# Kernel tuning notes

Hardware: AMD Instinct MI355X
Metric: run time of the kernel (lower is better)

Reference implementation:

```python
import jax, jax.numpy as jnp
import numpy as np

EPS = 1e-8  # torch F.cosine_similarity default eps


def setup_inputs() -> dict:
    key = jax.random.key(0)
    k1, k2 = jax.random.split(key)
    xs_pad = jax.random.normal(k1, (8, 8192, 256), dtype=jnp.float32)   # [B, T, D]
    spk_emb = jax.random.normal(k2, (8, 200, 256), dtype=jnp.float32)   # [B, S, D]
    return {"xs_pad": xs_pad, "spk_emb": spk_emb}


def reference(xs_pad, spk_emb):
    # Pairwise cosine similarity: [B, T, S]
    # Equivalent to F.cosine_similarity(xs.unsqueeze(2), spk.unsqueeze(1), dim=-1)
    # = dot(x, y) / max(||x|| * ||y||, eps)
    dot = jnp.einsum("btd,bsd->bts", xs_pad, spk_emb)
    nx = jnp.linalg.norm(xs_pad, axis=-1)    # [B, T]
    ny = jnp.linalg.norm(spk_emb, axis=-1)   # [B, S]
    denom = jnp.maximum(nx[:, :, None] * ny[:, None, :], EPS)
    return dot / denom
```

## Files before the change

### kernel.cpp

```cpp
#include <hip/hip_runtime.h>
#include <math.h>

typedef __attribute__((ext_vector_type(8))) _Float16 f16x8;
typedef __attribute__((ext_vector_type(4))) float f32x4;

#define BT 8192
#define BS 200
#define SP 208
#define DD 256
#define TM 128
#define LSTR 40
#define NJ 13

__global__ __launch_bounds__(256, 2)
void cos_scorer_kernel(const float* __restrict__ X, const float* __restrict__ SPK,
                       float* __restrict__ OUT) {
    const int b   = blockIdx.y;
    const int t0  = blockIdx.x * TM;
    const int tid = threadIdx.x;
    const int wid = tid >> 6;
    const int lane = tid & 63;
    const int lr  = lane & 15;
    const int lg  = lane >> 4;

    __shared__ _Float16 Shi[SP * LSTR];
    __shared__ _Float16 Slo[SP * LSTR];
    __shared__ float sn_l[SP];

    const float* __restrict__ spk_b = SPK + (size_t)b * BS * DD;

    const float* __restrict__ xrow0 = X + ((size_t)b * BT + t0 + wid * 32 + lr) * DD;
    const float* __restrict__ xrow1 = xrow0 + 16 * DD;

    float4 pa00 = *(const float4*)(xrow0 + lg * 8);
    float4 pa01 = *(const float4*)(xrow0 + lg * 8 + 4);
    float4 pa10 = *(const float4*)(xrow1 + lg * 8);
    float4 pa11 = *(const float4*)(xrow1 + lg * 8 + 4);

    if (tid < SP) {
        float ss = 0.f;
        if (tid < BS) {
            const float4* p = (const float4*)(spk_b + tid * DD);
            #pragma unroll 8
            for (int i = 0; i < DD / 4; ++i) {
                float4 v = p[i];
                ss = fmaf(v.x, v.x, ss); ss = fmaf(v.y, v.y, ss);
                ss = fmaf(v.z, v.z, ss); ss = fmaf(v.w, v.w, ss);
            }
        }
        sn_l[tid] = sqrtf(ss);
    }

    f32x4 acc[2][NJ];
    #pragma unroll
    for (int rt = 0; rt < 2; ++rt)
        #pragma unroll
        for (int j = 0; j < NJ; ++j)
            acc[rt][j] = (f32x4){0.f, 0.f, 0.f, 0.f};

    float ss0 = 0.f, ss1 = 0.f;

    for (int kb = 0; kb < 8; ++kb) {
        for (int i = tid; i < SP * 4; i += 256) {
            int s = i >> 2, part = i & 3;
            f16x8 hi, lo;
            #pragma unroll
            for (int e = 0; e < 8; ++e) { hi[e] = (_Float16)0.f; lo[e] = (_Float16)0.f; }
            if (s < BS) {
                const float* src = spk_b + s * DD + kb * 32 + part * 8;
                float4 v0 = *(const float4*)src;
                float4 v1 = *(const float4*)(src + 4);
                float xv[8] = {v0.x, v0.y, v0.z, v0.w, v1.x, v1.y, v1.z, v1.w};
                #pragma unroll
                for (int e = 0; e < 8; ++e) {
                    _Float16 h = (_Float16)xv[e];
                    hi[e] = h;
                    lo[e] = (_Float16)(xv[e] - (float)h);
                }
            }
            int off = s * LSTR + part * 8;
            *(f16x8*)&Shi[off] = hi;
            *(f16x8*)&Slo[off] = lo;
        }
        __syncthreads();

        f16x8 ahi0, alo0, ahi1, alo1;
        {
            float xv0[8] = {pa00.x, pa00.y, pa00.z, pa00.w, pa01.x, pa01.y, pa01.z, pa01.w};
            float xv1[8] = {pa10.x, pa10.y, pa10.z, pa10.w, pa11.x, pa11.y, pa11.z, pa11.w};
            #pragma unroll
            for (int e = 0; e < 8; ++e) {
                _Float16 h0 = (_Float16)xv0[e];
                ahi0[e] = h0; alo0[e] = (_Float16)(xv0[e] - (float)h0);
                ss0 = fmaf(xv0[e], xv0[e], ss0);
                _Float16 h1 = (_Float16)xv1[e];
                ahi1[e] = h1; alo1[e] = (_Float16)(xv1[e] - (float)h1);
                ss1 = fmaf(xv1[e], xv1[e], ss1);
            }
        }
        if (kb < 7) {
            int o = (kb + 1) * 32 + lg * 8;
            pa00 = *(const float4*)(xrow0 + o);
            pa01 = *(const float4*)(xrow0 + o + 4);
            pa10 = *(const float4*)(xrow1 + o);
            pa11 = *(const float4*)(xrow1 + o + 4);
        }

        #pragma unroll
        for (int j = 0; j < NJ; ++j) {
            int boff = (j * 16 + lr) * LSTR + lg * 8;
            f16x8 bhi = *(const f16x8*)&Shi[boff];
            f16x8 blo = *(const f16x8*)&Slo[boff];
            acc[0][j] = __builtin_amdgcn_mfma_f32_16x16x32_f16(ahi0, bhi, acc[0][j], 0, 0, 0);
            acc[1][j] = __builtin_amdgcn_mfma_f32_16x16x32_f16(ahi1, bhi, acc[1][j], 0, 0, 0);
            acc[0][j] = __builtin_amdgcn_mfma_f32_16x16x32_f16(alo0, bhi, acc[0][j], 0, 0, 0);
            acc[1][j] = __builtin_amdgcn_mfma_f32_16x16x32_f16(alo1, bhi, acc[1][j], 0, 0, 0);
            acc[0][j] = __builtin_amdgcn_mfma_f32_16x16x32_f16(ahi0, blo, acc[0][j], 0, 0, 0);
            acc[1][j] = __builtin_amdgcn_mfma_f32_16x16x32_f16(ahi1, blo, acc[1][j], 0, 0, 0);
        }
        __syncthreads();
    }

    ss0 += __shfl_xor(ss0, 16, 64);
    ss0 += __shfl_xor(ss0, 32, 64);
    ss1 += __shfl_xor(ss1, 16, 64);
    ss1 += __shfl_xor(ss1, 32, 64);

    #pragma unroll
    for (int rt = 0; rt < 2; ++rt) {
        float ssv = rt ? ss1 : ss0;
        #pragma unroll
        for (int reg = 0; reg < 4; ++reg) {
            int rc = lg * 4 + reg;
            float xn = sqrtf(__shfl(ssv, rc, 64));
            int row = t0 + wid * 32 + rt * 16 + rc;
            float* orow = OUT + ((size_t)b * BT + row) * BS;
            #pragma unroll
            for (int j = 0; j < NJ; ++j) {
                int col = j * 16 + lr;
                if (col < BS) {
                    float denom = fmaxf(xn * sn_l[col], 1e-8f);
                    orow[col] = acc[rt][j][reg] * __builtin_amdgcn_rcpf(denom);
                }
            }
        }
    }
}

extern "C" void kernel_launch(void* const* d_in, const int* in_sizes, int n_in,
                              void* d_out, int out_size, void* d_ws, size_t ws_size,
                              hipStream_t stream) {
    const float* X   = (const float*)d_in[0];
    const float* SPK = (const float*)d_in[1];
    float* OUT = (float*)d_out;

    dim3 grid(BT / TM, 8);
    dim3 block(256);
    hipLaunchKernelGGL(cos_scorer_kernel, grid, block, 0, stream, X, SPK, OUT);
}
```

Before: 138.5 us.

## Precompute speaker fp16 hi/lo fragments in workspace and drop LDS staging

Adds a prep kernel that splits speaker embeddings into fp16 hi/lo parts once per batch, stored in MFMA fragment order in the workspace, along with the speaker norms. The main kernel then reads B fragments straight from global/L2 instead of converting them redundantly in every block and staging through LDS with two barriers per k-step. Tiles shrink to 64 rows per block with higher occupancy. The cost is a second launch, more global/L2 traffic for B fragments, and a fallback path if the workspace is too small.

```diff
diff --git a/kernel.cpp b/kernel.cpp
--- a/kernel.cpp
+++ b/kernel.cpp
@@ -8,9 +8,138 @@
 #define BS 200
 #define SP 208
 #define DD 256
+#define NJ 13
+#define NKB 8
+
+#define SLOT_H 512
+#define PLANE_SLOTS (8 * NKB * NJ)
+#define PLANE_H ((size_t)PLANE_SLOTS * SLOT_H)
+#define WS_NEED (2 * PLANE_H * 2 + 8 * SP * 4)
+
+__global__ __launch_bounds__(256, 4)
+void spk_prep_kernel(const float* __restrict__ SPK, _Float16* __restrict__ wsH) {
+    const int j = blockIdx.x;
+    const int b = blockIdx.y;
+    const int tid = threadIdx.x;
+    const int w = tid >> 6;
+    const int lane = tid & 63;
+    const int lr = lane & 15;
+    const int lg = lane >> 4;
+    const int srow = j * 16 + lr;
+    const float* __restrict__ spk_b = SPK + (size_t)b * BS * DD;
+
+    __shared__ float pn[4][16];
+    float ss = 0.f;
+
+    #pragma unroll
+    for (int t = 0; t < 2; ++t) {
+        int kb = w + t * 4;
+        f16x8 hi, lo;
+        if (srow < BS) {
+            const float* src = spk_b + srow * DD + kb * 32 + lg * 8;
+            float4 v0 = *(const float4*)src;
+            float4 v1 = *(const float4*)(src + 4);
+            float xv[8] = {v0.x, v0.y, v0.z, v0.w, v1.x, v1.y, v1.z, v1.w};
+            #pragma unroll
+            for (int e = 0; e < 8; ++e) {
+                _Float16 h = (_Float16)xv[e];
+                hi[e] = h;
+                lo[e] = (_Float16)(xv[e] - (float)h);
+                ss = fmaf(xv[e], xv[e], ss);
+            }
+        } else {
+            #pragma unroll
+            for (int e = 0; e < 8; ++e) { hi[e] = (_Float16)0.f; lo[e] = (_Float16)0.f; }
+        }
+        size_t slot = ((size_t)(b * NKB + kb) * NJ + j) * SLOT_H + lane * 8;
+        *(f16x8*)&wsH[slot] = hi;
+        *(f16x8*)&wsH[PLANE_H + slot] = lo;
+    }
+
+    ss += __shfl_xor(ss, 16, 64);
+    ss += __shfl_xor(ss, 32, 64);
+    if (lane < 16) pn[w][lane] = ss;
+    __syncthreads();
+    if (tid < 16) {
+        float s = pn[0][tid] + pn[1][tid] + pn[2][tid] + pn[3][tid];
+        float* sn = (float*)(wsH + 2 * PLANE_H);
+        sn[b * SP + j * 16 + tid] = sqrtf(s);
+    }
+}
+
+__global__ __launch_bounds__(256, 4)
+void cos_main_kernel(const float* __restrict__ X, const _Float16* __restrict__ wsH,
+                     float* __restrict__ OUT) {
+    const int b   = blockIdx.y;
+    const int t0  = blockIdx.x * 64;
+    const int tid = threadIdx.x;
+    const int wid = tid >> 6;
+    const int lane = tid & 63;
+    const int lr = lane & 15;
+    const int lg = lane >> 4;
+
+    const float* __restrict__ xrow = X + ((size_t)b * BT + t0 + wid * 16 + lr) * DD;
+    const float* __restrict__ snW = (const float*)(wsH + 2 * PLANE_H) + b * SP;
+
+    float4 pa0 = *(const float4*)(xrow + lg * 8);
+    float4 pa1 = *(const float4*)(xrow + lg * 8 + 4);
+
+    f32x4 acc[NJ];
+    #pragma unroll
+    for (int j = 0; j < NJ; ++j) acc[j] = (f32x4){0.f, 0.f, 0.f, 0.f};
+    float ss = 0.f;
+
+    for (int kb = 0; kb < NKB; ++kb) {
+        f16x8 ahi, alo;
+        {
+            float xv[8] = {pa0.x, pa0.y, pa0.z, pa0.w, pa1.x, pa1.y, pa1.z, pa1.w};
+            #pragma unroll
+            for (int e = 0; e < 8; ++e) {
+                _Float16 h = (_Float16)xv[e];
+                ahi[e] = h;
+                alo[e] = (_Float16)(xv[e] - (float)h);
+                ss = fmaf(xv[e], xv[e], ss);
+            }
+        }
+        if (kb < NKB - 1) {
+            int o = (kb + 1) * 32 + lg * 8;
+            pa0 = *(const float4*)(xrow + o);
+            pa1 = *(const float4*)(xrow + o + 4);
+        }
+        const _Float16* __restrict__ base =
+            wsH + ((size_t)(b * NKB + kb) * NJ) * SLOT_H + lane * 8;
+        #pragma unroll
+        for (int j = 0; j < NJ; ++j) {
+            f16x8 bhi = *(const f16x8*)(base + (size_t)j * SLOT_H);
+            f16x8 blo = *(const f16x8*)(base + PLANE_H + (size_t)j * SLOT_H);
+            acc[j] = __builtin_amdgcn_mfma_f32_16x16x32_f16(ahi, bhi, acc[j], 0, 0, 0);
+            acc[j] = __builtin_amdgcn_mfma_f32_16x16x32_f16(alo, bhi, acc[j], 0, 0, 0);
+            acc[j] = __builtin_amdgcn_mfma_f32_16x16x32_f16(ahi, blo, acc[j], 0, 0, 0);
+        }
+    }
+
+    ss += __shfl_xor(ss, 16, 64);
+    ss += __shfl_xor(ss, 32, 64);
+
+    #pragma unroll
+    for (int reg = 0; reg < 4; ++reg) {
+        int rc = lg * 4 + reg;
+        float xn = sqrtf(__shfl(ss, rc, 64));
+        int row = t0 + wid * 16 + rc;
+        float* orow = OUT + ((size_t)b * BT + row) * BS;
+        #pragma unroll
+        for (int j = 0; j < NJ; ++j) {
+            int col = j * 16 + lr;
+            if (col < BS) {
+                float denom = fmaxf(xn * snW[col], 1e-8f);
+                orow[col] = acc[j][reg] * __builtin_amdgcn_rcpf(denom);
+            }
+        }
+    }
+}
+
 #define TM 128
 #define LSTR 40
-#define NJ 13
 
 __global__ __launch_bounds__(256, 2)
 void cos_scorer_kernel(const float* __restrict__ X, const float* __restrict__ SPK,
@@ -28,7 +157,6 @@
     __shared__ float sn_l[SP];
 
     const float* __restrict__ spk_b = SPK + (size_t)b * BS * DD;
-
     const float* __restrict__ xrow0 = X + ((size_t)b * BT + t0 + wid * 32 + lr) * DD;
     const float* __restrict__ xrow1 = xrow0 + 16 * DD;
 
@@ -154,7 +282,13 @@
     const float* SPK = (const float*)d_in[1];
     float* OUT = (float*)d_out;
 
-    dim3 grid(BT / TM, 8);
-    dim3 block(256);
-    hipLaunchKernelGGL(cos_scorer_kernel, grid, block, 0, stream, X, SPK, OUT);
-}
+    if (ws_size >= (size_t)WS_NEED) {
+        _Float16* wsH = (_Float16*)d_ws;
+        hipLaunchKernelGGL(spk_prep_kernel, dim3(NJ, 8), dim3(256), 0, stream, SPK, wsH);
+        hipLaunchKernelGGL(cos_main_kernel, dim3(BT / 64, 8), dim3(256), 0, stream,
+                           X, wsH, OUT);
+    } else {
+        hipLaunchKernelGGL(cos_scorer_kernel, dim3(BT / TM, 8), dim3(256), 0, stream,
+                           X, SPK, OUT);
+    }
+}
```

New measurement: 147.7 us. 1.07x slower.
